# Optimization experiments

Measured on AMD Instinct MI355X. Metric: run time of the kernel, lower is better.

## Reference

```python
import jax, jax.numpy as jnp
import numpy as np

NUM_USERS = 30000
NUM_ITEMS = 70000
N = NUM_USERS + NUM_ITEMS
D = 128
NNZ = 1_000_000
N_LAYERS = 3
BATCH = 16384
EPS = 1e-12  # torch F.normalize default eps
SLOPE = 0.01  # nn.LeakyReLU default negative_slope


def setup_inputs() -> dict:
    key = jax.random.key(0)
    ks = jax.random.split(key, 12)
    return {
        "userIdx": jax.random.randint(ks[0], (BATCH,), 0, NUM_USERS),
        "itemIdx": jax.random.randint(ks[1], (BATCH,), 0, NUM_ITEMS),
        "rows": jax.random.randint(ks[2], (NNZ,), 0, N),
        "cols": jax.random.randint(ks[3], (NNZ,), 0, N),
        "vals": jax.random.uniform(ks[4], (NNZ,), dtype=jnp.float32) * 0.1,
        "uEmbd": jax.random.normal(ks[5], (NUM_USERS, D), dtype=jnp.float32) * 0.1,
        "iEmbd": jax.random.normal(ks[6], (NUM_ITEMS, D), dtype=jnp.float32) * 0.1,
        "Wlin": jax.random.normal(ks[7], (N_LAYERS, D, D), dtype=jnp.float32) / np.sqrt(D),
        "blin": jax.random.normal(ks[8], (N_LAYERS, D), dtype=jnp.float32) * 0.01,
        "Wint": jax.random.normal(ks[9], (N_LAYERS, D, D), dtype=jnp.float32) / np.sqrt(D),
        "bint": jax.random.normal(ks[10], (N_LAYERS, D), dtype=jnp.float32) * 0.01,
    }


def reference(userIdx, itemIdx, rows, cols, vals, uEmbd, iEmbd, Wlin, blin, Wint, bint):
    num_users = uEmbd.shape[0]
    n = uEmbd.shape[0] + iEmbd.shape[0]
    features = jnp.concatenate([uEmbd, iEmbd], axis=0)  # [N, D]
    embds = [features]
    for l in range(Wlin.shape[0]):
        # SpMM: L @ features via gather + segment_sum over COO edges
        Lx = jax.ops.segment_sum(vals[:, None] * features[cols], rows, num_segments=n)
        # (L + I) @ f then linear
        part1 = (Lx + features) @ Wlin[l] + blin[l]
        # (L @ f) * f then linear
        part2 = (Lx * features) @ Wint[l] + bint[l]
        features = jax.nn.leaky_relu(part1 + part2, negative_slope=SLOPE)
        norm = jnp.maximum(jnp.linalg.norm(features, axis=1, keepdims=True), EPS)
        features = features / norm
        embds.append(features)
    finalEmbd = jnp.concatenate(embds, axis=1)  # [N, D*(1+n_layers)]
    u = finalEmbd[userIdx]
    i = finalEmbd[itemIdx + num_users]
    return jnp.sum(u * i, axis=1)
```

## Files before the change

kernel.cpp:

```cpp
#include <hip/hip_runtime.h>
#include <hip/hip_bf16.h>

#define NU 30000
#define NI 70000
#define NN 100000
#define DD 128
#define NLAYERS 3
#define SLOPE_ 0.01f
#define EPS_ 1e-12f

#define NB 782
#define NBKT 1024
#define NBLK 256
#define AROW 136
#define MAXL 32768
#define BM 64

typedef __bf16 v8bf __attribute__((ext_vector_type(8)));
typedef float v16f __attribute__((ext_vector_type(16)));
typedef float v2f __attribute__((ext_vector_type(2)));
typedef unsigned short ushort_t;

union UB8 { uint4 u; v8bf v; };

__device__ __forceinline__ float bflo(unsigned u) { return __uint_as_float(u << 16); }
__device__ __forceinline__ float bfhi(unsigned u) { return __uint_as_float(u & 0xffff0000u); }

__device__ __forceinline__ unsigned pk2(float a, float b) {
    __hip_bfloat162 h = __float22bfloat162_rn(make_float2(a, b));
    return *reinterpret_cast<unsigned*>(&h);
}
__device__ __forceinline__ uint4 pk8(const float* f) {
    return make_uint4(pk2(f[0], f[1]), pk2(f[2], f[3]), pk2(f[4], f[5]), pk2(f[6], f[7]));
}
__device__ __forceinline__ void unp8(uint4 g, float* f) {
    f[0] = bflo(g.x); f[1] = bfhi(g.x);
    f[2] = bflo(g.y); f[3] = bfhi(g.y);
    f[4] = bflo(g.z); f[5] = bfhi(g.z);
    f[6] = bflo(g.w); f[7] = bfhi(g.w);
}
__device__ __forceinline__ ushort_t f2bf1(float x) {
    __hip_bfloat16 h = __float2bfloat16(x);
    return *reinterpret_cast<ushort_t*>(&h);
}

__global__ __launch_bounds__(256) void k_concat_bf(const float* __restrict__ u,
                                                   const float* __restrict__ it,
                                                   ushort_t* __restrict__ fb) {
    int idx = blockIdx.x * 256 + threadIdx.x;
    if (idx >= NN * DD / 8) return;
    size_t base = (size_t)idx * 8;
    const float* src = (base < (size_t)NU * DD) ? (u + base) : (it + base - (size_t)NU * DD);
    float f[8];
    float4 a = *(const float4*)src;
    float4 b = *(const float4*)(src + 4);
    f[0] = a.x; f[1] = a.y; f[2] = a.z; f[3] = a.w;
    f[4] = b.x; f[5] = b.y; f[6] = b.z; f[7] = b.w;
    *(uint4*)(fb + base) = pk8(f);
}

__device__ __forceinline__ void dot_body(const ushort_t* __restrict__ fb,
                                         const int* __restrict__ uIdx,
                                         const int* __restrict__ iIdx,
                                         float* __restrict__ out,
                                         int batch, int accum, int blk, int t) {
    int b = blk * 4 + (t >> 6);
    if (b >= batch) return;
    int lane = t & 63;
    unsigned ua = *(const unsigned*)(fb + (size_t)uIdx[b] * DD + lane * 2);
    unsigned ib = *(const unsigned*)(fb + (size_t)(iIdx[b] + NU) * DD + lane * 2);
    float s = bflo(ua) * bflo(ib) + bfhi(ua) * bfhi(ib);
#pragma unroll
    for (int m = 32; m; m >>= 1) s += __shfl_xor(s, m, 64);
    if (lane == 0) out[b] = accum ? out[b] + s : s;
}

__global__ __launch_bounds__(256) void k_dot(const ushort_t* __restrict__ fb,
                                             const int* __restrict__ uIdx,
                                             const int* __restrict__ iIdx,
                                             float* __restrict__ out,
                                             int batch, int accum) {
    dot_body(fb, uIdx, iIdx, out, batch, accum, blockIdx.x, threadIdx.x);
}

__global__ __launch_bounds__(1024) void k_lhist(const int* __restrict__ rows,
                                                int* __restrict__ ghist,
                                                int* __restrict__ flags,
                                                int nnz, int epb) {
    __shared__ int h[NBKT];
    int t = threadIdx.x, b = blockIdx.x;
    h[t] = 0;
    int i0 = b * 1024 + t;
    if (i0 < NN) flags[i0] = 0;
    __syncthreads();
    int e0 = b * epb, e1 = min(e0 + epb, nnz);
    for (int e = e0 + t; e < e1; e += 1024) atomicAdd(&h[rows[e] >> 7], 1);
    __syncthreads();
    ghist[t * NBLK + b] = h[t];
}

__global__ __launch_bounds__(256) void k_rscan(int* __restrict__ ghist,
                                               int* __restrict__ btot,
                                               const int* __restrict__ uIdx,
                                               const int* __restrict__ iIdx,
                                               int* __restrict__ flags,
                                               int* __restrict__ cnt, int batch) {
    int t = threadIdx.x;
    int gid = blockIdx.x * 256 + t;
    if (gid == 0) *cnt = 0;
    if (gid < batch) flags[uIdx[gid]] = 1;
    else if (gid < 2 * batch) flags[iIdx[gid - batch] + NU] = 1;

    int bkt = blockIdx.x * 4 + (t >> 6);
    int lane = t & 63;
    int* row = ghist + bkt * NBLK;
    int4 c = *(const int4*)(row + lane * 4);
    int s = c.x + c.y + c.z + c.w;
    int incl = s;
#pragma unroll
    for (int m = 1; m < 64; m <<= 1) {
        int o = __shfl_up(incl, m, 64);
        if (lane >= m) incl += o;
    }
    int excl = incl - s;
    int4 o;
    o.x = excl;
    o.y = o.x + c.x;
    o.z = o.y + c.y;
    o.w = o.z + c.z;
    *(int4*)(row + lane * 4) = o;
    if (lane == 63) btot[bkt] = incl;
}

__global__ __launch_bounds__(256) void k_btscan(const int* __restrict__ btot,
                                                int* __restrict__ bbase) {
    int t = threadIdx.x;
    int4 c = *(const int4*)(btot + t * 4);
    int tsum = c.x + c.y + c.z + c.w;
    int incl = tsum;
#pragma unroll
    for (int m = 1; m < 64; m <<= 1) {
        int o = __shfl_up(incl, m, 64);
        if ((t & 63) >= m) incl += o;
    }
    __shared__ int wsum[4];
    if ((t & 63) == 63) wsum[t >> 6] = incl;
    __syncthreads();
    int off = 0;
    for (int i = 0; i < (t >> 6); ++i) off += wsum[i];
    int excl = off + incl - tsum;
    int4 o;
    o.x = excl;
    o.y = o.x + c.x;
    o.z = o.y + c.y;
    o.w = o.z + c.z;
    *(int4*)(bbase + t * 4) = o;
    if (t == 255) bbase[NBKT] = o.w + c.w;
}

__global__ __launch_bounds__(1024) void k_sscatter(const int* __restrict__ rows,
                                                   const int* __restrict__ cols,
                                                   const float* __restrict__ vals,
                                                   const int* __restrict__ ghist,
                                                   const int* __restrict__ bbase,
                                                   int2* __restrict__ bedges,
                                                   const int* __restrict__ flags,
                                                   int* __restrict__ list,
                                                   int* __restrict__ cnt,
                                                   int nnz, int epb) {
    __shared__ int base[NBKT];
    __shared__ int h[NBKT];
    int t = threadIdx.x, b = blockIdx.x;
    base[t] = bbase[t] + ghist[t * NBLK + b];
    h[t] = 0;
    int lane = t & 63;
    int i = b * 1024 + t;
    int f = (i < NN) ? flags[i] : 0;
    unsigned long long mask = __ballot(f);
    int total = __popcll(mask);
    int prefix = __popcll(mask & ((1ULL << lane) - 1));
    int bs = 0;
    if (lane == 0 && total) bs = atomicAdd(cnt, total);
    bs = __shfl(bs, 0, 64);
    if (f) list[bs + prefix] = i;
    __syncthreads();
    int e0 = b * epb, e1 = min(e0 + epb, nnz);
    for (int e = e0 + t; e < e1; e += 1024) {
        int r = rows[e];
        int bkt = r >> 7;
        int rank = atomicAdd(&h[bkt], 1);
        bedges[base[bkt] + rank] = make_int2(((r & 127) << 20) | cols[e],
                                             __float_as_int(vals[e]));
    }
}

__global__ __launch_bounds__(256) void k_csort(const int* __restrict__ bbase,
                                               const int2* __restrict__ bedges,
                                               int2* __restrict__ edges,
                                               int* __restrict__ rowPtr, int nnz) {
    __shared__ int cntS[128];
    __shared__ int fillS[128];
    __shared__ int wtot;
    int b = blockIdx.x, t = threadIdx.x;
    int s0 = bbase[b];
    int s1 = bbase[b + 1];
    if (t < 128) cntS[t] = 0;
    __syncthreads();
    for (int i = s0 + t; i < s1; i += 256) atomicAdd(&cntS[bedges[i].x >> 20], 1);
    __syncthreads();
    int v = 0, incl = 0;
    if (t < 128) {
        v = cntS[t];
        incl = v;
#pragma unroll
        for (int m = 1; m < 64; m <<= 1) {
            int o = __shfl_up(incl, m, 64);
            if ((t & 63) >= m) incl += o;
        }
        if (t == 63) wtot = incl;
    }
    __syncthreads();
    if (t < 128) {
        int excl = incl - v + ((t >= 64) ? wtot : 0);
        fillS[t] = excl;
        int gr = b * 128 + t;
        if (gr < NN) rowPtr[gr] = s0 + excl;
    }
    if (b == 0 && t == 0) rowPtr[NN] = nnz;
    __syncthreads();
    for (int i = s0 + t; i < s1; i += 256) {
        int2 e = bedges[i];
        int r = e.x >> 20;
        int p = atomicAdd(&fillS[r], 1);
        edges[s0 + p] = make_int2(e.x & 0xFFFFF, e.y);
    }
}

__global__ __launch_bounds__(256) void k_wprep(const float* __restrict__ Wlin,
                                               const float* __restrict__ Wint,
                                               uint4* __restrict__ Wb4) {
    int id = blockIdx.x * 256 + threadIdx.x;
    int lane = id & 63;
    int w = (id >> 6) & 3;
    int s = (id >> 8) & 7;
    int c = (id >> 11) & 1;
    int l = id >> 12;
    const float* src = (c ? Wint : Wlin) + (size_t)l * DD * DD;
    int n = w * 32 + (lane & 31);
    int k0 = s * 16 + ((lane >> 5) & 1) * 8;
    float f[8];
#pragma unroll
    for (int j = 0; j < 8; ++j) f[j] = src[(size_t)(k0 + j) * DD + n];
    Wb4[id] = pk8(f);
}

__device__ __forceinline__ void acc_pk(v2f* acc2, uint4 g, float v) {
    v2f vv = {v, v};
    unsigned gw[4] = {g.x, g.y, g.z, g.w};
#pragma unroll
    for (int p = 0; p < 4; ++p) {
        v2f x = {bflo(gw[p]), bfhi(gw[p])};
        acc2[p] = x * vv + acc2[p];
    }
}

__device__ __forceinline__ void spmm_quarter(int r, bool valid, int t,
                                             const int* __restrict__ rowPtr,
                                             const int2* __restrict__ edges,
                                             const ushort_t* __restrict__ fb,
                                             ushort_t* __restrict__ Lxb) {
    int d0 = (t & 15) * 8;
    int beg = 0, end = 0;
    if (valid) { beg = rowPtr[r]; end = rowPtr[r + 1]; }
    v2f acc2[4];
#pragma unroll
    for (int p = 0; p < 4; ++p) acc2[p] = (v2f){0.f, 0.f};
    int e = beg;
    for (; e + 3 < end; e += 4) {
        int2 p0 = edges[e];
        int2 p1 = edges[e + 1];
        int2 p2 = edges[e + 2];
        int2 p3 = edges[e + 3];
        uint4 g0 = *(const uint4*)(fb + (size_t)p0.x * DD + d0);
        uint4 g1 = *(const uint4*)(fb + (size_t)p1.x * DD + d0);
        uint4 g2 = *(const uint4*)(fb + (size_t)p2.x * DD + d0);
        uint4 g3 = *(const uint4*)(fb + (size_t)p3.x * DD + d0);
        acc_pk(acc2, g0, __int_as_float(p0.y));
        acc_pk(acc2, g1, __int_as_float(p1.y));
        acc_pk(acc2, g2, __int_as_float(p2.y));
        acc_pk(acc2, g3, __int_as_float(p3.y));
    }
    if (e + 1 < end) {
        int2 p0 = edges[e];
        int2 p1 = edges[e + 1];
        uint4 g0 = *(const uint4*)(fb + (size_t)p0.x * DD + d0);
        uint4 g1 = *(const uint4*)(fb + (size_t)p1.x * DD + d0);
        acc_pk(acc2, g0, __int_as_float(p0.y));
        acc_pk(acc2, g1, __int_as_float(p1.y));
        e += 2;
    }
    if (e < end) {
        int2 p0 = edges[e];
        uint4 g0 = *(const uint4*)(fb + (size_t)p0.x * DD + d0);
        acc_pk(acc2, g0, __int_as_float(p0.y));
    }
    if (valid) {
        float acc[8];
#pragma unroll
        for (int p = 0; p < 4; ++p) { acc[2 * p] = acc2[p][0]; acc[2 * p + 1] = acc2[p][1]; }
        *(uint4*)(Lxb + (size_t)r * DD + d0) = pk8(acc);
    }
}

__global__ __launch_bounds__(256) void k_spmm_dot(const int* __restrict__ rowPtr,
                                                  const int2* __restrict__ edges,
                                                  const ushort_t* __restrict__ fb,
                                                  ushort_t* __restrict__ Lxb,
                                                  const int* __restrict__ uIdx,
                                                  const int* __restrict__ iIdx,
                                                  float* __restrict__ out,
                                                  int batch, int accum, int dotBlocks) {
    if ((int)blockIdx.x < dotBlocks) {
        dot_body(fb, uIdx, iIdx, out, batch, accum, blockIdx.x, threadIdx.x);
        return;
    }
    int ridx = (blockIdx.x - dotBlocks) * 16 + (threadIdx.x >> 4);
    spmm_quarter(ridx, ridx < NN, threadIdx.x, rowPtr, edges, fb, Lxb);
}

__global__ __launch_bounds__(256) void k_spmm_idx_dot(const int* __restrict__ rowPtr,
                                                      const int2* __restrict__ edges,
                                                      const ushort_t* __restrict__ fb,
                                                      ushort_t* __restrict__ Lxb,
                                                      const int* __restrict__ list,
                                                      const int* __restrict__ cnt,
                                                      const int* __restrict__ uIdx,
                                                      const int* __restrict__ iIdx,
                                                      float* __restrict__ out,
                                                      int batch, int dotBlocks) {
    if ((int)blockIdx.x < dotBlocks) {
        dot_body(fb, uIdx, iIdx, out, batch, 1, blockIdx.x, threadIdx.x);
        return;
    }
    int i = (blockIdx.x - dotBlocks) * 16 + (threadIdx.x >> 4);
    bool valid = i < *cnt;
    int r = valid ? list[i] : 0;
    spmm_quarter(r, valid, threadIdx.x, rowPtr, edges, fb, Lxb);
}

template <bool INDEXED>
__device__ __forceinline__ void layer_body(const ushort_t* __restrict__ Lxb,
                                           const uint4* __restrict__ Wb4,
                                           const float* __restrict__ blin,
                                           const float* __restrict__ bint,
                                           ushort_t* __restrict__ fb,
                                           const ushort_t* __restrict__ fin,
                                           const int* __restrict__ list, int nc) {
    __shared__ ushort_t As[2][BM * AROW];
    __shared__ float pnormAll[BM * 4];
    __shared__ float rinvS[BM];
    __shared__ int rowIdS[BM];

    const int t = threadIdx.x;
    const int w = t >> 6;
    const int l = t & 63;
    const int q = l >> 5;
    const int ln = l & 31;
    const int n = w * 32 + ln;
    const int m0 = blockIdx.x * BM;

    if (INDEXED && m0 >= nc) return;

    if (t < BM) {
        int gi = m0 + t;
        int gm;
        if (INDEXED) gm = (gi < nc) ? list[gi] : -1;
        else gm = (gi < NN) ? gi : -1;
        rowIdS[t] = gm;
    }
    __syncthreads();

    const float bias = blin[n] + bint[n];

    v16f acc[2];
#pragma unroll
    for (int mt = 0; mt < 2; ++mt)
#pragma unroll
        for (int i = 0; i < 16; ++i) acc[mt][i] = 0.f;

#pragma unroll
    for (int ii = 0; ii < 4; ++ii) {
        int idx = ii * 256 + t;
        int row = idx >> 4;
        int ch = idx & 15;
        int gm = rowIdS[row];
        uint4 sv = make_uint4(0, 0, 0, 0);
        uint4 pv = make_uint4(0, 0, 0, 0);
        if (gm >= 0) {
            uint4 gl = *(const uint4*)(Lxb + (size_t)gm * DD + ch * 8);
            uint4 gf = *(const uint4*)(fin + (size_t)gm * DD + ch * 8);
            float a[8], b[8], r[8];
            unp8(gl, a);
            unp8(gf, b);
#pragma unroll
            for (int j = 0; j < 8; ++j) r[j] = a[j] + b[j];
            sv = pk8(r);
#pragma unroll
            for (int j = 0; j < 8; ++j) r[j] = a[j] * b[j];
            pv = pk8(r);
        }
        *(uint4*)&As[0][row * AROW + ch * 8] = sv;
        *(uint4*)&As[1][row * AROW + ch * 8] = pv;
    }
    __syncthreads();

#pragma unroll
    for (int c = 0; c < 2; ++c) {
        UB8 bf[8];
#pragma unroll
        for (int s = 0; s < 8; ++s) bf[s].u = Wb4[c * 2048 + s * 256 + w * 64 + l];
#pragma unroll
        for (int mt = 0; mt < 2; ++mt) {
#pragma unroll
            for (int s = 0; s < 8; ++s) {
                v8bf af = *(const v8bf*)&As[c][(mt * 32 + ln) * AROW + s * 16 + q * 8];
                acc[mt] = __builtin_amdgcn_mfma_f32_32x32x16_bf16(af, bf[s].v, acc[mt], 0, 0, 0);
            }
        }
    }

#pragma unroll
    for (int mt = 0; mt < 2; ++mt) {
        float r[16];
#pragma unroll
        for (int reg = 0; reg < 16; ++reg) {
            float v = acc[mt][reg] + bias;
            v = (v > 0.f) ? v : SLOPE_ * v;
            acc[mt][reg] = v;
            r[reg] = v * v;
        }
#pragma unroll
        for (int lev = 0; lev < 4; ++lev) {
            int m = 1 << lev;
            int cnt2 = 8 >> lev;
            bool hi = (l & m) != 0;
#pragma unroll
            for (int i = 0; i < 8; ++i) {
                if (i < cnt2) {
                    float p = hi ? r[2 * i + 1] : r[2 * i];
                    float qv = hi ? r[2 * i] : r[2 * i + 1];
                    r[i] = p + __shfl_xor(qv, m, 64);
                }
            }
        }
        float tot = r[0] + __shfl_xor(r[0], 16, 64);
        if ((l & 31) < 16) {
            int i = l & 15;
            int row = (i & 3) + ((i >> 2) << 3) + 4 * q;
            pnormAll[(mt * 32 + row) * 4 + w] = tot;
        }
    }
    __syncthreads();
    if (t < BM) {
        float4 p = *(const float4*)&pnormAll[t * 4];
        float tot = p.x + p.y + p.z + p.w;
        rinvS[t] = 1.0f / fmaxf(sqrtf(tot), EPS_);
    }
    __syncthreads();

#pragma unroll
    for (int mt = 0; mt < 2; ++mt) {
#pragma unroll
        for (int reg = 0; reg < 16; ++reg) {
            int row = (reg & 3) + ((reg >> 2) << 3) + 4 * q;
            int gm = rowIdS[mt * 32 + row];
            if (gm >= 0)
                fb[(size_t)gm * DD + n] = f2bf1(acc[mt][reg] * rinvS[mt * 32 + row]);
        }
    }
}

__global__ __launch_bounds__(256, 4) void k_layer2(const ushort_t* __restrict__ Lxb,
                                                   const uint4* __restrict__ Wb4,
                                                   const float* __restrict__ blin,
                                                   const float* __restrict__ bint,
                                                   const ushort_t* __restrict__ fin,
                                                   ushort_t* __restrict__ fb) {
    layer_body<false>(Lxb, Wb4, blin, bint, fb, fin, nullptr, 0);
}

__global__ __launch_bounds__(256, 4) void k_layer_idx(const ushort_t* __restrict__ Lxb,
                                                      const uint4* __restrict__ Wb4,
                                                      const float* __restrict__ blin,
                                                      const float* __restrict__ bint,
                                                      const ushort_t* __restrict__ fin,
                                                      ushort_t* __restrict__ fb,
                                                      const int* __restrict__ list,
                                                      const int* __restrict__ cnt) {
    layer_body<true>(Lxb, Wb4, blin, bint, fb, fin, list, *cnt);
}

extern "C" void kernel_launch(void* const* d_in, const int* in_sizes, int n_in,
                              void* d_out, int out_size, void* d_ws, size_t ws_size,
                              hipStream_t stream) {
    const int*   userIdx = (const int*)d_in[0];
    const int*   itemIdx = (const int*)d_in[1];
    const int*   rows    = (const int*)d_in[2];
    const int*   cols    = (const int*)d_in[3];
    const float* vals    = (const float*)d_in[4];
    const float* uE      = (const float*)d_in[5];
    const float* iE      = (const float*)d_in[6];
    const float* Wlin    = (const float*)d_in[7];
    const float* blin    = (const float*)d_in[8];
    const float* Wint    = (const float*)d_in[9];
    const float* bint    = (const float*)d_in[10];
    float* out = (float*)d_out;

    const int batch = in_sizes[0];
    const int nnz   = in_sizes[2];
    const int epb   = (nnz + NBLK - 1) / NBLK;
    const int dotBlocks = (batch + 3) / 4;

    ushort_t* featA = (ushort_t*)d_ws;
    ushort_t* featB = featA + (size_t)NN * DD;
    ushort_t* Lxb   = featB + (size_t)NN * DD;
    uint4* Wb4      = (uint4*)(Lxb + (size_t)NN * DD);
    int2*  bedges   = (int2*)(Wb4 + 12288);
    int2*  edges    = bedges + nnz;
    int*   ghist    = (int*)(edges + nnz);
    int*   btot     = ghist + NBKT * NBLK;
    int*   bbase    = btot + NBKT;
    int*   rowPtr   = bbase + NBKT + 4;
    int*   flags    = rowPtr + NN + 4;
    int*   list     = flags + NN;
    int*   cnt      = list + MAXL;

    k_concat_bf<<<(NN * DD / 8 + 255) / 256, 256, 0, stream>>>(uE, iE, featA);
    k_wprep<<<48, 256, 0, stream>>>(Wlin, Wint, Wb4);

    k_lhist<<<NBLK, 1024, 0, stream>>>(rows, ghist, flags, nnz, epb);
    k_rscan<<<NBKT / 4, 256, 0, stream>>>(ghist, btot, userIdx, itemIdx, flags, cnt, batch);
    k_btscan<<<1, 256, 0, stream>>>(btot, bbase);
    k_sscatter<<<NBLK, 1024, 0, stream>>>(rows, cols, vals, ghist, bbase, bedges,
                                          flags, list, cnt, nnz, epb);
    k_csort<<<NB, 256, 0, stream>>>(bbase, bedges, edges, rowPtr, nnz);

    k_spmm_dot<<<dotBlocks + (NN + 15) / 16, 256, 0, stream>>>(
        rowPtr, edges, featA, Lxb, userIdx, itemIdx, out, batch, 0, dotBlocks);
    k_layer2<<<(NN + BM - 1) / BM, 256, 0, stream>>>(
        Lxb, Wb4, blin, bint, featA, featB);

    k_spmm_dot<<<dotBlocks + (NN + 15) / 16, 256, 0, stream>>>(
        rowPtr, edges, featB, Lxb, userIdx, itemIdx, out, batch, 1, dotBlocks);
    k_layer2<<<(NN + BM - 1) / BM, 256, 0, stream>>>(
        Lxb, Wb4 + 4096, blin + DD, bint + DD, featB, featA);

    k_spmm_idx_dot<<<dotBlocks + (MAXL + 15) / 16, 256, 0, stream>>>(
        rowPtr, edges, featA, Lxb, list, cnt, userIdx, itemIdx, out, batch, dotBlocks);
    k_layer_idx<<<(MAXL + BM - 1) / BM, 256, 0, stream>>>(
        Lxb, Wb4 + 8192, blin + 2 * DD, bint + 2 * DD, featA, featB, list, cnt);

    k_dot<<<dotBlocks, 256, 0, stream>>>(featB, userIdx, itemIdx, out, batch, 1);
}
```

Before: 335.7 us.

## Fuse SpMM gather into layer GEMM kernel, removing Lx intermediate buffer

Merges the per-layer SpMM and dense layer kernels into a single 512-thread kernel. Each block first gathers neighbor rows for its 64 output rows directly into shared memory as (Lx+f) and (Lx*f) bf16 tiles, then runs the MFMA GEMM. Each of 8 waves now handles one 32-row M tile. This removes the Lx global write and reread and one launch per layer. In exchange, the irregular gather and the GEMM now share one block, which can cost latency hiding and occupancy.

```diff
diff --git a/kernel.cpp b/kernel.cpp
--- a/kernel.cpp
+++ b/kernel.cpp
@@ -59,14 +59,12 @@
     *(uint4*)(fb + base) = pk8(f);
 }
 
-__device__ __forceinline__ void dot_body(const ushort_t* __restrict__ fb,
+__device__ __forceinline__ void dot_wave(const ushort_t* __restrict__ fb,
                                          const int* __restrict__ uIdx,
                                          const int* __restrict__ iIdx,
                                          float* __restrict__ out,
-                                         int batch, int accum, int blk, int t) {
-    int b = blk * 4 + (t >> 6);
+                                         int batch, int accum, int b, int lane) {
     if (b >= batch) return;
-    int lane = t & 63;
     unsigned ua = *(const unsigned*)(fb + (size_t)uIdx[b] * DD + lane * 2);
     unsigned ib = *(const unsigned*)(fb + (size_t)(iIdx[b] + NU) * DD + lane * 2);
     float s = bflo(ua) * bflo(ib) + bfhi(ua) * bfhi(ib);
@@ -80,7 +78,8 @@
                                              const int* __restrict__ iIdx,
                                              float* __restrict__ out,
                                              int batch, int accum) {
-    dot_body(fb, uIdx, iIdx, out, batch, accum, blockIdx.x, threadIdx.x);
+    dot_wave(fb, uIdx, iIdx, out, batch, accum,
+             blockIdx.x * 4 + (threadIdx.x >> 6), threadIdx.x & 63);
 }
 
 __global__ __launch_bounds__(1024) void k_lhist(const int* __restrict__ rows,
@@ -264,98 +263,16 @@
     }
 }
 
-__device__ __forceinline__ void spmm_quarter(int r, bool valid, int t,
-                                             const int* __restrict__ rowPtr,
-                                             const int2* __restrict__ edges,
-                                             const ushort_t* __restrict__ fb,
-                                             ushort_t* __restrict__ Lxb) {
-    int d0 = (t & 15) * 8;
-    int beg = 0, end = 0;
-    if (valid) { beg = rowPtr[r]; end = rowPtr[r + 1]; }
-    v2f acc2[4];
-#pragma unroll
-    for (int p = 0; p < 4; ++p) acc2[p] = (v2f){0.f, 0.f};
-    int e = beg;
-    for (; e + 3 < end; e += 4) {
-        int2 p0 = edges[e];
-        int2 p1 = edges[e + 1];
-        int2 p2 = edges[e + 2];
-        int2 p3 = edges[e + 3];
-        uint4 g0 = *(const uint4*)(fb + (size_t)p0.x * DD + d0);
-        uint4 g1 = *(const uint4*)(fb + (size_t)p1.x * DD + d0);
-        uint4 g2 = *(const uint4*)(fb + (size_t)p2.x * DD + d0);
-        uint4 g3 = *(const uint4*)(fb + (size_t)p3.x * DD + d0);
-        acc_pk(acc2, g0, __int_as_float(p0.y));
-        acc_pk(acc2, g1, __int_as_float(p1.y));
-        acc_pk(acc2, g2, __int_as_float(p2.y));
-        acc_pk(acc2, g3, __int_as_float(p3.y));
-    }
-    if (e + 1 < end) {
-        int2 p0 = edges[e];
-        int2 p1 = edges[e + 1];
-        uint4 g0 = *(const uint4*)(fb + (size_t)p0.x * DD + d0);
-        uint4 g1 = *(const uint4*)(fb + (size_t)p1.x * DD + d0);
-        acc_pk(acc2, g0, __int_as_float(p0.y));
-        acc_pk(acc2, g1, __int_as_float(p1.y));
-        e += 2;
-    }
-    if (e < end) {
-        int2 p0 = edges[e];
-        uint4 g0 = *(const uint4*)(fb + (size_t)p0.x * DD + d0);
-        acc_pk(acc2, g0, __int_as_float(p0.y));
-    }
-    if (valid) {
-        float acc[8];
-#pragma unroll
-        for (int p = 0; p < 4; ++p) { acc[2 * p] = acc2[p][0]; acc[2 * p + 1] = acc2[p][1]; }
-        *(uint4*)(Lxb + (size_t)r * DD + d0) = pk8(acc);
-    }
-}
-
-__global__ __launch_bounds__(256) void k_spmm_dot(const int* __restrict__ rowPtr,
-                                                  const int2* __restrict__ edges,
-                                                  const ushort_t* __restrict__ fb,
-                                                  ushort_t* __restrict__ Lxb,
-                                                  const int* __restrict__ uIdx,
-                                                  const int* __restrict__ iIdx,
-                                                  float* __restrict__ out,
-                                                  int batch, int accum, int dotBlocks) {
-    if ((int)blockIdx.x < dotBlocks) {
-        dot_body(fb, uIdx, iIdx, out, batch, accum, blockIdx.x, threadIdx.x);
-        return;
-    }
-    int ridx = (blockIdx.x - dotBlocks) * 16 + (threadIdx.x >> 4);
-    spmm_quarter(ridx, ridx < NN, threadIdx.x, rowPtr, edges, fb, Lxb);
-}
-
-__global__ __launch_bounds__(256) void k_spmm_idx_dot(const int* __restrict__ rowPtr,
-                                                      const int2* __restrict__ edges,
-                                                      const ushort_t* __restrict__ fb,
-                                                      ushort_t* __restrict__ Lxb,
-                                                      const int* __restrict__ list,
-                                                      const int* __restrict__ cnt,
-                                                      const int* __restrict__ uIdx,
-                                                      const int* __restrict__ iIdx,
-                                                      float* __restrict__ out,
-                                                      int batch, int dotBlocks) {
-    if ((int)blockIdx.x < dotBlocks) {
-        dot_body(fb, uIdx, iIdx, out, batch, 1, blockIdx.x, threadIdx.x);
-        return;
-    }
-    int i = (blockIdx.x - dotBlocks) * 16 + (threadIdx.x >> 4);
-    bool valid = i < *cnt;
-    int r = valid ? list[i] : 0;
-    spmm_quarter(r, valid, threadIdx.x, rowPtr, edges, fb, Lxb);
-}
-
 template <bool INDEXED>
-__device__ __forceinline__ void layer_body(const ushort_t* __restrict__ Lxb,
-                                           const uint4* __restrict__ Wb4,
-                                           const float* __restrict__ blin,
-                                           const float* __restrict__ bint,
-                                           ushort_t* __restrict__ fb,
-                                           const ushort_t* __restrict__ fin,
-                                           const int* __restrict__ list, int nc) {
+__device__ __forceinline__ void flayer_body(int bid,
+                                            const int* __restrict__ rowPtr,
+                                            const int2* __restrict__ edges,
+                                            const uint4* __restrict__ Wb4,
+                                            const float* __restrict__ blin,
+                                            const float* __restrict__ bint,
+                                            const ushort_t* __restrict__ fin,
+                                            ushort_t* __restrict__ fout,
+                                            const int* __restrict__ list, int nc) {
     __shared__ ushort_t As[2][BM * AROW];
     __shared__ float pnormAll[BM * 4];
     __shared__ float rinvS[BM];
@@ -364,10 +281,12 @@
     const int t = threadIdx.x;
     const int w = t >> 6;
     const int l = t & 63;
+    const int mt = w >> 2;
+    const int w2 = w & 3;
     const int q = l >> 5;
     const int ln = l & 31;
-    const int n = w * 32 + ln;
-    const int m0 = blockIdx.x * BM;
+    const int n = w2 * 32 + ln;
+    const int m0 = bid * BM;
 
     if (INDEXED && m0 >= nc) return;
 
@@ -380,124 +299,176 @@
     }
     __syncthreads();
 
+    {
+        const int qi = t >> 4;
+        const int d0 = (t & 15) * 8;
+#pragma unroll
+        for (int j = 0; j < 2; ++j) {
+            int row = qi * 2 + j;
+            int gm = rowIdS[row];
+            uint4 sv = make_uint4(0, 0, 0, 0);
+            uint4 pv = make_uint4(0, 0, 0, 0);
+            if (gm >= 0) {
+                int beg = rowPtr[gm], end = rowPtr[gm + 1];
+                v2f acc2[4];
+#pragma unroll
+                for (int p = 0; p < 4; ++p) acc2[p] = (v2f){0.f, 0.f};
+                int e = beg;
+                for (; e + 3 < end; e += 4) {
+                    int2 p0 = edges[e];
+                    int2 p1 = edges[e + 1];
+                    int2 p2 = edges[e + 2];
+                    int2 p3 = edges[e + 3];
+                    uint4 g0 = *(const uint4*)(fin + (size_t)p0.x * DD + d0);
+                    uint4 g1 = *(const uint4*)(fin + (size_t)p1.x * DD + d0);
+                    uint4 g2 = *(const uint4*)(fin + (size_t)p2.x * DD + d0);
+                    uint4 g3 = *(const uint4*)(fin + (size_t)p3.x * DD + d0);
+                    acc_pk(acc2, g0, __int_as_float(p0.y));
+                    acc_pk(acc2, g1, __int_as_float(p1.y));
+                    acc_pk(acc2, g2, __int_as_float(p2.y));
+                    acc_pk(acc2, g3, __int_as_float(p3.y));
+                }
+                if (e + 1 < end) {
+                    int2 p0 = edges[e];
+                    int2 p1 = edges[e + 1];
+                    uint4 g0 = *(const uint4*)(fin + (size_t)p0.x * DD + d0);
+                    uint4 g1 = *(const uint4*)(fin + (size_t)p1.x * DD + d0);
+                    acc_pk(acc2, g0, __int_as_float(p0.y));
+                    acc_pk(acc2, g1, __int_as_float(p1.y));
+                    e += 2;
+                }
+                if (e < end) {
+                    int2 p0 = edges[e];
+                    uint4 g0 = *(const uint4*)(fin + (size_t)p0.x * DD + d0);
+                    acc_pk(acc2, g0, __int_as_float(p0.y));
+                }
+                float a[8], b8[8], r8[8];
+#pragma unroll
+                for (int p = 0; p < 4; ++p) {
+                    a[2 * p] = acc2[p][0];
+                    a[2 * p + 1] = acc2[p][1];
+                }
+                uint4 gf = *(const uint4*)(fin + (size_t)gm * DD + d0);
+                unp8(gf, b8);
+#pragma unroll
+                for (int k = 0; k < 8; ++k) r8[k] = a[k] + b8[k];
+                sv = pk8(r8);
+#pragma unroll
+                for (int k = 0; k < 8; ++k) r8[k] = a[k] * b8[k];
+                pv = pk8(r8);
+            }
+            *(uint4*)&As[0][row * AROW + d0] = sv;
+            *(uint4*)&As[1][row * AROW + d0] = pv;
+        }
+    }
+    __syncthreads();
+
     const float bias = blin[n] + bint[n];
-
-    v16f acc[2];
-#pragma unroll
-    for (int mt = 0; mt < 2; ++mt)
-#pragma unroll
-        for (int i = 0; i < 16; ++i) acc[mt][i] = 0.f;
-
-#pragma unroll
-    for (int ii = 0; ii < 4; ++ii) {
-        int idx = ii * 256 + t;
-        int row = idx >> 4;
-        int ch = idx & 15;
-        int gm = rowIdS[row];
-        uint4 sv = make_uint4(0, 0, 0, 0);
-        uint4 pv = make_uint4(0, 0, 0, 0);
-        if (gm >= 0) {
-            uint4 gl = *(const uint4*)(Lxb + (size_t)gm * DD + ch * 8);
-            uint4 gf = *(const uint4*)(fin + (size_t)gm * DD + ch * 8);
-            float a[8], b[8], r[8];
-            unp8(gl, a);
-            unp8(gf, b);
-#pragma unroll
-            for (int j = 0; j < 8; ++j) r[j] = a[j] + b[j];
-            sv = pk8(r);
-#pragma unroll
-            for (int j = 0; j < 8; ++j) r[j] = a[j] * b[j];
-            pv = pk8(r);
-        }
-        *(uint4*)&As[0][row * AROW + ch * 8] = sv;
-        *(uint4*)&As[1][row * AROW + ch * 8] = pv;
-    }
-    __syncthreads();
+    v16f acc;
+#pragma unroll
+    for (int i = 0; i < 16; ++i) acc[i] = 0.f;
 
 #pragma unroll
     for (int c = 0; c < 2; ++c) {
-        UB8 bf[8];
-#pragma unroll
-        for (int s = 0; s < 8; ++s) bf[s].u = Wb4[c * 2048 + s * 256 + w * 64 + l];
-#pragma unroll
-        for (int mt = 0; mt < 2; ++mt) {
-#pragma unroll
-            for (int s = 0; s < 8; ++s) {
-                v8bf af = *(const v8bf*)&As[c][(mt * 32 + ln) * AROW + s * 16 + q * 8];
-                acc[mt] = __builtin_amdgcn_mfma_f32_32x32x16_bf16(af, bf[s].v, acc[mt], 0, 0, 0);
+#pragma unroll
+        for (int sh = 0; sh < 2; ++sh) {
+            UB8 bf[4];
+#pragma unroll
+            for (int k = 0; k < 4; ++k)
+                bf[k].u = Wb4[c * 2048 + (sh * 4 + k) * 256 + w2 * 64 + l];
+#pragma unroll
+            for (int k = 0; k < 4; ++k) {
+                v8bf af = *(const v8bf*)&As[c][(mt * 32 + ln) * AROW + (sh * 4 + k) * 16 + q * 8];
+                acc = __builtin_amdgcn_mfma_f32_32x32x16_bf16(af, bf[k].v, acc, 0, 0, 0);
             }
         }
     }
 
-#pragma unroll
-    for (int mt = 0; mt < 2; ++mt) {
-        float r[16];
-#pragma unroll
-        for (int reg = 0; reg < 16; ++reg) {
-            float v = acc[mt][reg] + bias;
-            v = (v > 0.f) ? v : SLOPE_ * v;
-            acc[mt][reg] = v;
-            r[reg] = v * v;
-        }
-#pragma unroll
-        for (int lev = 0; lev < 4; ++lev) {
-            int m = 1 << lev;
-            int cnt2 = 8 >> lev;
-            bool hi = (l & m) != 0;
-#pragma unroll
-            for (int i = 0; i < 8; ++i) {
-                if (i < cnt2) {
-                    float p = hi ? r[2 * i + 1] : r[2 * i];
-                    float qv = hi ? r[2 * i] : r[2 * i + 1];
-                    r[i] = p + __shfl_xor(qv, m, 64);
-                }
+    float r[16];
+#pragma unroll
+    for (int reg = 0; reg < 16; ++reg) {
+        float v = acc[reg] + bias;
+        v = (v > 0.f) ? v : SLOPE_ * v;
+        acc[reg] = v;
+        r[reg] = v * v;
+    }
+#pragma unroll
+    for (int lev = 0; lev < 4; ++lev) {
+        int m = 1 << lev;
+        int cnt2 = 8 >> lev;
+        bool hi = (l & m) != 0;
+#pragma unroll
+        for (int i = 0; i < 8; ++i) {
+            if (i < cnt2) {
+                float p = hi ? r[2 * i + 1] : r[2 * i];
+                float qv = hi ? r[2 * i] : r[2 * i + 1];
+                r[i] = p + __shfl_xor(qv, m, 64);
             }
         }
-        float tot = r[0] + __shfl_xor(r[0], 16, 64);
-        if ((l & 31) < 16) {
-            int i = l & 15;
-            int row = (i & 3) + ((i >> 2) << 3) + 4 * q;
-            pnormAll[(mt * 32 + row) * 4 + w] = tot;
-        }
+    }
+    float tot = r[0] + __shfl_xor(r[0], 16, 64);
+    if ((l & 31) < 16) {
+        int i = l & 15;
+        int row = (i & 3) + ((i >> 2) << 3) + 4 * q;
+        pnormAll[(mt * 32 + row) * 4 + w2] = tot;
     }
     __syncthreads();
     if (t < BM) {
         float4 p = *(const float4*)&pnormAll[t * 4];
-        float tot = p.x + p.y + p.z + p.w;
-        rinvS[t] = 1.0f / fmaxf(sqrtf(tot), EPS_);
-    }
-    __syncthreads();
-
-#pragma unroll
-    for (int mt = 0; mt < 2; ++mt) {
-#pragma unroll
-        for (int reg = 0; reg < 16; ++reg) {
-            int row = (reg & 3) + ((reg >> 2) << 3) + 4 * q;
-            int gm = rowIdS[mt * 32 + row];
-            if (gm >= 0)
-                fb[(size_t)gm * DD + n] = f2bf1(acc[mt][reg] * rinvS[mt * 32 + row]);
-        }
-    }
-}
-
-__global__ __launch_bounds__(256, 4) void k_layer2(const ushort_t* __restrict__ Lxb,
+        float s = p.x + p.y + p.z + p.w;
+        rinvS[t] = 1.0f / fmaxf(sqrtf(s), EPS_);
+    }
+    __syncthreads();
+
+#pragma unroll
+    for (int reg = 0; reg < 16; ++reg) {
+        int row = (reg & 3) + ((reg >> 2) << 3) + 4 * q;
+        int gm = rowIdS[mt * 32 + row];
+        if (gm >= 0)
+            fout[(size_t)gm * DD + n] = f2bf1(acc[reg] * rinvS[mt * 32 + row]);
+    }
+}
+
+__global__ __launch_bounds__(512, 8) void k_flayer(const int* __restrict__ rowPtr,
+                                                   const int2* __restrict__ edges,
                                                    const uint4* __restrict__ Wb4,
                                                    const float* __restrict__ blin,
                                                    const float* __restrict__ bint,
                                                    const ushort_t* __restrict__ fin,
-                                                   ushort_t* __restrict__ fb) {
-    layer_body<false>(Lxb, Wb4, blin, bint, fb, fin, nullptr, 0);
-}
-
-__global__ __launch_bounds__(256, 4) void k_layer_idx(const ushort_t* __restrict__ Lxb,
-                                                      const uint4* __restrict__ Wb4,
-                                                      const float* __restrict__ blin,
-                                                      const float* __restrict__ bint,
-                                                      const ushort_t* __restrict__ fin,
-                                                      ushort_t* __restrict__ fb,
-                                                      const int* __restrict__ list,
-                                                      const int* __restrict__ cnt) {
-    layer_body<true>(Lxb, Wb4, blin, bint, fb, fin, list, *cnt);
+                                                   ushort_t* __restrict__ fout,
+                                                   const int* __restrict__ uIdx,
+                                                   const int* __restrict__ iIdx,
+                                                   float* __restrict__ out,
+                                                   int batch, int accum, int dotBlocks) {
+    if ((int)blockIdx.x < dotBlocks) {
+        dot_wave(fin, uIdx, iIdx, out, batch, accum,
+                 blockIdx.x * 8 + (threadIdx.x >> 6), threadIdx.x & 63);
+        return;
+    }
+    flayer_body<false>(blockIdx.x - dotBlocks, rowPtr, edges, Wb4, blin, bint,
+                       fin, fout, nullptr, 0);
+}
+
+__global__ __launch_bounds__(512, 8) void k_flayer_idx(const int* __restrict__ rowPtr,
+                                                       const int2* __restrict__ edges,
+                                                       const uint4* __restrict__ Wb4,
+                                                       const float* __restrict__ blin,
+                                                       const float* __restrict__ bint,
+                                                       const ushort_t* __restrict__ fin,
+                                                       ushort_t* __restrict__ fout,
+                                                       const int* __restrict__ list,
+                                                       const int* __restrict__ cnt,
+                                                       const int* __restrict__ uIdx,
+                                                       const int* __restrict__ iIdx,
+                                                       float* __restrict__ out,
+                                                       int batch, int dotBlocks) {
+    if ((int)blockIdx.x < dotBlocks) {
+        dot_wave(fin, uIdx, iIdx, out, batch, 1,
+                 blockIdx.x * 8 + (threadIdx.x >> 6), threadIdx.x & 63);
+        return;
+    }
+    flayer_body<true>(blockIdx.x - dotBlocks, rowPtr, edges, Wb4, blin, bint,
+                      fin, fout, list, *cnt);
 }
 
 extern "C" void kernel_launch(void* const* d_in, const int* in_sizes, int n_in,
@@ -519,12 +490,12 @@
     const int batch = in_sizes[0];
     const int nnz   = in_sizes[2];
     const int epb   = (nnz + NBLK - 1) / NBLK;
-    const int dotBlocks = (batch + 3) / 4;
+    const int dotB8 = (batch + 7) / 8;
+    const int dotB4 = (batch + 3) / 4;
 
     ushort_t* featA = (ushort_t*)d_ws;
     ushort_t* featB = featA + (size_t)NN * DD;
-    ushort_t* Lxb   = featB + (size_t)NN * DD;
-    uint4* Wb4      = (uint4*)(Lxb + (size_t)NN * DD);
+    uint4* Wb4      = (uint4*)(featB + (size_t)NN * DD);
     int2*  bedges   = (int2*)(Wb4 + 12288);
     int2*  edges    = bedges + nnz;
     int*   ghist    = (int*)(edges + nnz);
@@ -545,20 +516,17 @@
                                           flags, list, cnt, nnz, epb);
     k_csort<<<NB, 256, 0, stream>>>(bbase, bedges, edges, rowPtr, nnz);
 
-    k_spmm_dot<<<dotBlocks + (NN + 15) / 16, 256, 0, stream>>>(
-        rowPtr, edges, featA, Lxb, userIdx, itemIdx, out, batch, 0, dotBlocks);
-    k_layer2<<<(NN + BM - 1) / BM, 256, 0, stream>>>(
-        Lxb, Wb4, blin, bint, featA, featB);
-
-    k_spmm_dot<<<dotBlocks + (NN + 15) / 16, 256, 0, stream>>>(
-        rowPtr, edges, featB, Lxb, userIdx, itemIdx, out, batch, 1, dotBlocks);
-    k_layer2<<<(NN + BM - 1) / BM, 256, 0, stream>>>(
-        Lxb, Wb4 + 4096, blin + DD, bint + DD, featB, featA);
-
-    k_spmm_idx_dot<<<dotBlocks + (MAXL + 15) / 16, 256, 0, stream>>>(
-        rowPtr, edges, featA, Lxb, list, cnt, userIdx, itemIdx, out, batch, dotBlocks);
-    k_layer_idx<<<(MAXL + BM - 1) / BM, 256, 0, stream>>>(
-        Lxb, Wb4 + 8192, blin + 2 * DD, bint + 2 * DD, featA, featB, list, cnt);
-
-    k_dot<<<dotBlocks, 256, 0, stream>>>(featB, userIdx, itemIdx, out, batch, 1);
-}
+    k_flayer<<<dotB8 + (NN + BM - 1) / BM, 512, 0, stream>>>(
+        rowPtr, edges, Wb4, blin, bint, featA, featB,
+        userIdx, itemIdx, out, batch, 0, dotB8);
+
+    k_flayer<<<dotB8 + (NN + BM - 1) / BM, 512, 0, stream>>>(
+        rowPtr, edges, Wb4 + 4096, blin + DD, bint + DD, featB, featA,
+        userIdx, itemIdx, out, batch, 1, dotB8);
+
+    k_flayer_idx<<<dotB8 + (MAXL + BM - 1) / BM, 512, 0, stream>>>(
+        rowPtr, edges, Wb4 + 8192, blin + 2 * DD, bint + 2 * DD, featA, featB,
+        list, cnt, userIdx, itemIdx, out, batch, dotB8);
+
+    k_dot<<<dotB4, 256, 0, stream>>>(featB, userIdx, itemIdx, out, batch, 1);
+}
```

After: 314.1 us. 1.07x faster.
